# Performance work log

Hardware: AMD Instinct MI355X
Metric: run time of the kernel (lower is better)

The kernel has to match this reference:

```python
import jax, jax.numpy as jnp
import numpy as np


def _decode(out, anchors, t, case, thresh):
    # out: [B, 3*D, H, W] -> [B, H, W, 3, D]; D = 5 + n_classes
    B, C, H, W = out.shape
    o = jnp.transpose(out, (0, 2, 3, 1)).reshape(B, H, W, 3, C // 3)
    mask = o[..., 0] > thresh  # objectness logit threshold (pre-sigmoid, as in original)
    dt = out.dtype
    gx = jnp.arange(W, dtype=dt)  # grid x runs along W (index[:,2] in original)
    gy = jnp.arange(H, dtype=dt)  # grid y runs along H (index[:,1] in original)
    scale = t / case
    cx = (gx[None, None, :, None] + o[..., 1]) * scale
    cy = (gy[None, :, None, None] + o[..., 2]) * scale
    w = anchors[None, None, None, :, 0] * jnp.exp(o[..., 3]) / case
    h = anchors[None, None, None, :, 1] * jnp.exp(o[..., 4]) / case
    p = jax.nn.sigmoid(o[..., 0])
    cls_idx = jnp.argmax(o[..., 5:], axis=-1).astype(dt)
    boxes = jnp.stack([p, cx, cy, w, h, cls_idx], axis=-1).reshape(-1, 6)
    return boxes, mask.reshape(-1)


def setup_inputs() -> dict:
    key = jax.random.key(0)
    k13, k26, k52, kt = jax.random.split(key, 4)
    B = 32
    inp = {
        "output_13": jax.random.normal(k13, (B, 255, 13, 13), dtype=jnp.float32),
        "output_26": jax.random.normal(k26, (B, 255, 26, 26), dtype=jnp.float32),
        "output_52": jax.random.normal(k52, (B, 255, 52, 52), dtype=jnp.float32),
        # canonical YOLOv3 pixel anchors per scale
        "anchors_13": jnp.array([[116.0, 90.0], [156.0, 198.0], [373.0, 326.0]], dtype=jnp.float32),
        "anchors_26": jnp.array([[30.0, 61.0], [62.0, 45.0], [59.0, 119.0]], dtype=jnp.float32),
        "anchors_52": jnp.array([[10.0, 13.0], [16.0, 30.0], [33.0, 23.0]], dtype=jnp.float32),
        "thresh": jnp.array([0.5], dtype=jnp.float32),
        "case": 416,
    }
    return inp


def reference(output_13, output_26, output_52, anchors_13, anchors_26, anchors_52, thresh, case):
    th = thresh[0]
    b13, m13 = _decode(output_13, anchors_13, 32.0, case, th)
    b26, m26 = _decode(output_26, anchors_26, 16.0, case, th)
    b52, m52 = _decode(output_52, anchors_52, 8.0, case, th)
    boxes = jnp.concatenate([b13, b26, b52], axis=0)  # [N_total, 6], row-major (b,h,w,a) per scale
    mask = jnp.concatenate([m13, m26, m52], axis=0)   # boxes[mask] == original torch.cat output
    return boxes, mask
```

## Files before the change

kernel.cpp:

```cpp
#include <hip/hip_runtime.h>


#define NCLS 80

template<int HW, int W>
__device__ __forceinline__ void decode4(
    const float* __restrict__ in, const float* __restrict__ anch,
    float scale, float inv_case, float th,
    int a, int t, int row_base, int B,
    float* __restrict__ boxes, float* __restrict__ mask)
{
    if (t >= B * HW * 4) return;
    const int rt  = t >> 2;
    const int seg = t & 3;
    const int b   = rt / HW;
    const int hw  = rt - b * HW;

    const float* p = in + ((size_t)b * 255 + (size_t)a * 85) * HW + hw;

    const float* pc = p + (size_t)(5 + seg * 20) * HW;
    float v[20];
#pragma unroll
    for (int j = 0; j < 20; ++j)
        v[j] = __builtin_nontemporal_load(&pc[(size_t)j * HW]);

    float best = v[0];
    int   bi   = seg * 20;
#pragma unroll
    for (int j = 1; j < 20; ++j)
        if (v[j] > best) { best = v[j]; bi = seg * 20 + j; }

    float o0 = __builtin_nontemporal_load(&p[0 * (size_t)HW]);
    float o1 = __builtin_nontemporal_load(&p[1 * (size_t)HW]);
    float o2 = __builtin_nontemporal_load(&p[2 * (size_t)HW]);
    float o3 = __builtin_nontemporal_load(&p[3 * (size_t)HW]);
    float o4 = __builtin_nontemporal_load(&p[4 * (size_t)HW]);

#pragma unroll
    for (int m = 1; m <= 2; m <<= 1) {
        float ob = __shfl_xor(best, m);
        int   oi = __shfl_xor(bi,   m);
        if (ob > best || (ob == best && oi < bi)) { best = ob; bi = oi; }
    }

    if (seg == 0) {
        int h = hw / W;
        int w = hw - h * W;
        float px = 1.0f / (1.0f + __expf(-o0));
        float cx = ((float)w + o1) * scale;
        float cy = ((float)h + o2) * scale;
        float bw = anch[2 * a + 0] * __expf(o3) * inv_case;
        float bh = anch[2 * a + 1] * __expf(o4) * inv_case;

        int row = row_base + rt * 3 + a;
        float2* ob2 = reinterpret_cast<float2*>(boxes + (size_t)row * 6);
        ob2[0] = make_float2(px, cx);
        ob2[1] = make_float2(cy, bw);
        ob2[2] = make_float2(bh, (float)bi);
        mask[row] = (o0 > th) ? 1.0f : 0.0f;
    }
}

__global__ __launch_bounds__(256) void detector_kernel(
    const float* __restrict__ in13, const float* __restrict__ in26,
    const float* __restrict__ in52,
    const float* __restrict__ a13, const float* __restrict__ a26,
    const float* __restrict__ a52,
    const float* __restrict__ thp, const int* __restrict__ casep,
    float* __restrict__ boxes, float* __restrict__ mask,
    int B, int nb52, int nb26)
{
    const int a  = blockIdx.y;
    const int bx = blockIdx.x;
    const float th       = thp[0];
    const float inv_case = 1.0f / (float)casep[0];

    if (bx < nb52) {
        int t = bx * 256 + threadIdx.x;
        decode4<2704, 52>(in52, a52, 8.0f * inv_case, inv_case, th,
                          a, t, B * (169 + 676) * 3, B, boxes, mask);
    } else if (bx < nb52 + nb26) {
        int t = (bx - nb52) * 256 + threadIdx.x;
        decode4<676, 26>(in26, a26, 16.0f * inv_case, inv_case, th,
                         a, t, B * 169 * 3, B, boxes, mask);
    } else {
        int t = (bx - nb52 - nb26) * 256 + threadIdx.x;
        decode4<169, 13>(in13, a13, 32.0f * inv_case, inv_case, th,
                         a, t, 0, B, boxes, mask);
    }
}

extern "C" void kernel_launch(void* const* d_in, const int* in_sizes, int n_in,
                              void* d_out, int out_size, void* d_ws, size_t ws_size,
                              hipStream_t stream) {
    const float* in13 = (const float*)d_in[0];
    const float* in26 = (const float*)d_in[1];
    const float* in52 = (const float*)d_in[2];
    const float* a13  = (const float*)d_in[3];
    const float* a26  = (const float*)d_in[4];
    const float* a52  = (const float*)d_in[5];
    const float* thp  = (const float*)d_in[6];
    const int*   casep = (const int*)d_in[7];

    const int B = in_sizes[0] / (255 * 169);

    const int nb52 = (B * 2704 * 4 + 255) / 256;
    const int nb26 = (B * 676  * 4 + 255) / 256;
    const int nb13 = (B * 169  * 4 + 255) / 256;

    const int nrows = B * (169 + 676 + 2704) * 3;
    float* boxes = (float*)d_out;
    float* mask  = (float*)d_out + (size_t)nrows * 6;

    dim3 grid(nb52 + nb26 + nb13, 3);
    detector_kernel<<<grid, 256, 0, stream>>>(
        in13, in26, in52, a13, a26, a52, thp, casep,
        boxes, mask, B, nb52, nb26);
}
```

Before: 171.5 us.

## Split 52-scale decode into vectorized partial-argmax and merge kernels

Restructures the work into two kernels. The first computes per-class-chunk argmax partials for the 52 scale using float4 loads, writes them to workspace, and also fully decodes the 26 scale (with a shared-memory merge) and the 13 scale. The second kernel merges the four 52-scale partials and writes the boxes. The aim is wider, better-coalesced loads and more parallelism across class chunks, at the cost of an extra launch and a workspace round trip. Nontemporal loads are also dropped.

```diff
diff --git a/kernel.cpp b/kernel.cpp
--- a/kernel.cpp
+++ b/kernel.cpp
@@ -1,15 +1,146 @@
 #include <hip/hip_runtime.h>
 
 
-#define NCLS 80
-
-template<int HW, int W>
-__device__ __forceinline__ void decode4(
+typedef float vf4 __attribute__((ext_vector_type(4)));
+
+#define UPD1(B,I,V,C) { if ((V) > (B)) { (B)=(V); (I)=(C); } }
+#define UPD4(bb,ii,vv,cc) \
+    UPD1(bb.x, ii.x, vv.x, cc) UPD1(bb.y, ii.y, vv.y, cc) \
+    UPD1(bb.z, ii.z, vv.z, cc) UPD1(bb.w, ii.w, vv.w, cc)
+#define MRG1(B,I,V,C) { if ((V) > (B) || ((V)==(B) && (C) < (I))) { (B)=(V); (I)=(C); } }
+#define MRG4(bb,ii,vv,cc) \
+    MRG1(bb.x, ii.x, vv.x, cc.x) MRG1(bb.y, ii.y, vv.y, cc.y) \
+    MRG1(bb.z, ii.z, vv.z, cc.z) MRG1(bb.w, ii.w, vv.w, cc.w)
+
+__device__ __forceinline__ void store_p(float2* pb, int col, vf4 b, int4 i) {
+    vf4* p = reinterpret_cast<vf4*>(pb + (size_t)col * 4);
+    vf4 lo = {b.x, (float)i.x, b.y, (float)i.y};
+    vf4 hi = {b.z, (float)i.z, b.w, (float)i.w};
+    p[0] = lo; p[1] = hi;
+}
+
+__device__ __forceinline__ void p1_chunk52(
+    const float* __restrict__ in52, float2* __restrict__ partial, int u)
+{
+    const int slice = u >> 2;
+    const int k     = u & 3;
+    const int t     = threadIdx.x;
+    const vf4* __restrict__ cp = reinterpret_cast<const vf4*>(
+        in52 + (size_t)slice * 85 * 2704 + (size_t)(5 + 20 * k) * 2704);
+
+    const bool a2 = (t < 164);
+    const int base = 20 * k;
+
+    vf4 b0 = cp[t], b1 = cp[256 + t];
+    vf4 b2 = a2 ? cp[512 + t] : b0;
+    int4 i0 = {base, base, base, base}, i1 = i0, i2 = i0;
+
+    vf4 n0 = cp[676 + t], n1 = cp[676 + 256 + t];
+    vf4 n2 = a2 ? cp[676 + 512 + t] : n0;
+
+#pragma unroll 2
+    for (int c = 1; c < 19; ++c) {
+        const vf4* ch = cp + (size_t)(c + 1) * 676;
+        vf4 m0 = ch[t], m1 = ch[256 + t];
+        vf4 m2 = a2 ? ch[512 + t] : m0;
+        const int cls = base + c;
+        UPD4(b0, i0, n0, cls) UPD4(b1, i1, n1, cls) UPD4(b2, i2, n2, cls)
+        n0 = m0; n1 = m1; n2 = m2;
+    }
+    UPD4(b0, i0, n0, base + 19) UPD4(b1, i1, n1, base + 19) UPD4(b2, i2, n2, base + 19)
+
+    float2* pb = partial + (size_t)u * 2704;
+    store_p(pb, t, b0, i0);
+    store_p(pb, 256 + t, b1, i1);
+    if (a2) store_p(pb, 512 + t, b2, i2);
+}
+
+__device__ __forceinline__ void p1_full26(
+    const float* __restrict__ in26, const float* __restrict__ anch,
+    float scale, float inv_case, float th, int slice, int rb26,
+    float* __restrict__ boxes, float* __restrict__ mask,
+    vf4* __restrict__ lbest, int4* __restrict__ lbi)
+{
+    const int t = threadIdx.x;
+    const int b = slice / 3, a = slice - b * 3;
+    const vf4* __restrict__ sp = reinterpret_cast<const vf4*>(in26)
+                               + (size_t)slice * 85 * 169;
+    const vf4* __restrict__ cp = sp + 5 * 169;
+
+    const bool a2 = (t < 164);
+    const int p0 = t,        k40 = p0 / 169, c0 = p0 - k40 * 169;
+    const int p1 = 256 + t,  k41 = p1 / 169, c1 = p1 - k41 * 169;
+    const int p2 = 512 + t,  k42 = p2 / 169, c2 = p2 - k42 * 169;
+    (void)c0; (void)c1; (void)c2;
+
+    vf4 b0 = cp[p0], b1 = cp[p1];
+    vf4 b2 = a2 ? cp[p2] : b0;
+    int4 i0 = {k40, k40, k40, k40}, i1 = {k41, k41, k41, k41}, i2 = {k42, k42, k42, k42};
+
+    vf4 n0 = cp[676 + p0], n1 = cp[676 + p1];
+    vf4 n2 = a2 ? cp[676 + p2] : n0;
+
+#pragma unroll 2
+    for (int g = 1; g < 19; ++g) {
+        const vf4* gp = cp + (size_t)(g + 1) * 676;
+        vf4 m0 = gp[p0], m1 = gp[p1];
+        vf4 m2 = a2 ? gp[p2] : m0;
+        const int g4 = 4 * g;
+        UPD4(b0, i0, n0, g4 + k40) UPD4(b1, i1, n1, g4 + k41) UPD4(b2, i2, n2, g4 + k42)
+        n0 = m0; n1 = m1; n2 = m2;
+    }
+    UPD4(b0, i0, n0, 76 + k40) UPD4(b1, i1, n1, 76 + k41) UPD4(b2, i2, n2, 76 + k42)
+
+    lbest[p0] = b0; lbi[p0] = i0;
+    lbest[p1] = b1; lbi[p1] = i1;
+    if (a2) { lbest[p2] = b2; lbi[p2] = i2; }
+    __syncthreads();
+
+    if (t < 169) {
+        vf4 bb = lbest[t]; int4 ii = lbi[t];
+#pragma unroll
+        for (int k4 = 1; k4 < 4; ++k4) {
+            vf4 vb = lbest[k4 * 169 + t]; int4 vi = lbi[k4 * 169 + t];
+            MRG4(bb, ii, vb, vi)
+        }
+        vf4 o0 = sp[t], o1 = sp[169 + t], o2 = sp[2 * 169 + t];
+        vf4 o3 = sp[3 * 169 + t], o4 = sp[4 * 169 + t];
+        const float A0 = anch[2 * a + 0], A1 = anch[2 * a + 1];
+        const float e0[4] = {o0.x, o0.y, o0.z, o0.w};
+        const float e1[4] = {o1.x, o1.y, o1.z, o1.w};
+        const float e2[4] = {o2.x, o2.y, o2.z, o2.w};
+        const float e3[4] = {o3.x, o3.y, o3.z, o3.w};
+        const float e4[4] = {o4.x, o4.y, o4.z, o4.w};
+        const int   bi[4] = {ii.x, ii.y, ii.z, ii.w};
+        const float bv[4] = {bb.x, bb.y, bb.z, bb.w};
+        (void)bv;
+#pragma unroll
+        for (int e = 0; e < 4; ++e) {
+            const int hw = t * 4 + e;
+            const int hh = hw / 26;
+            const int ww = hw - hh * 26;
+            const float px = 1.f / (1.f + __expf(-e0[e]));
+            const float cx = ((float)ww + e1[e]) * scale;
+            const float cy = ((float)hh + e2[e]) * scale;
+            const float bw = A0 * __expf(e3[e]) * inv_case;
+            const float bh = A1 * __expf(e4[e]) * inv_case;
+            const int row = rb26 + (b * 676 + hw) * 3 + a;
+            float2* ob2 = reinterpret_cast<float2*>(boxes + (size_t)row * 6);
+            ob2[0] = make_float2(px, cx);
+            ob2[1] = make_float2(cy, bw);
+            ob2[2] = make_float2(bh, (float)bi[e]);
+            mask[row] = (e0[e] > th) ? 1.0f : 0.0f;
+        }
+    }
+}
+
+__device__ __forceinline__ void decode4_13(
     const float* __restrict__ in, const float* __restrict__ anch,
     float scale, float inv_case, float th,
-    int a, int t, int row_base, int B,
+    int a, int t, int B,
     float* __restrict__ boxes, float* __restrict__ mask)
 {
+    constexpr int HW = 169, W = 13;
     if (t >= B * HW * 4) return;
     const int rt  = t >> 2;
     const int seg = t & 3;
@@ -17,12 +148,10 @@
     const int hw  = rt - b * HW;
 
     const float* p = in + ((size_t)b * 255 + (size_t)a * 85) * HW + hw;
-
     const float* pc = p + (size_t)(5 + seg * 20) * HW;
     float v[20];
 #pragma unroll
-    for (int j = 0; j < 20; ++j)
-        v[j] = __builtin_nontemporal_load(&pc[(size_t)j * HW]);
+    for (int j = 0; j < 20; ++j) v[j] = pc[(size_t)j * HW];
 
     float best = v[0];
     int   bi   = seg * 20;
@@ -30,11 +159,8 @@
     for (int j = 1; j < 20; ++j)
         if (v[j] > best) { best = v[j]; bi = seg * 20 + j; }
 
-    float o0 = __builtin_nontemporal_load(&p[0 * (size_t)HW]);
-    float o1 = __builtin_nontemporal_load(&p[1 * (size_t)HW]);
-    float o2 = __builtin_nontemporal_load(&p[2 * (size_t)HW]);
-    float o3 = __builtin_nontemporal_load(&p[3 * (size_t)HW]);
-    float o4 = __builtin_nontemporal_load(&p[4 * (size_t)HW]);
+    float o0 = p[0 * (size_t)HW], o1 = p[1 * (size_t)HW], o2 = p[2 * (size_t)HW];
+    float o3 = p[3 * (size_t)HW], o4 = p[4 * (size_t)HW];
 
 #pragma unroll
     for (int m = 1; m <= 2; m <<= 1) {
@@ -44,15 +170,13 @@
     }
 
     if (seg == 0) {
-        int h = hw / W;
-        int w = hw - h * W;
-        float px = 1.0f / (1.0f + __expf(-o0));
-        float cx = ((float)w + o1) * scale;
-        float cy = ((float)h + o2) * scale;
-        float bw = anch[2 * a + 0] * __expf(o3) * inv_case;
-        float bh = anch[2 * a + 1] * __expf(o4) * inv_case;
-
-        int row = row_base + rt * 3 + a;
+        const int h = hw / W, w = hw - (hw / W) * W;
+        const float px = 1.0f / (1.0f + __expf(-o0));
+        const float cx = ((float)w + o1) * scale;
+        const float cy = ((float)h + o2) * scale;
+        const float bw = anch[2 * a + 0] * __expf(o3) * inv_case;
+        const float bh = anch[2 * a + 1] * __expf(o4) * inv_case;
+        const int row = rt * 3 + a;
         float2* ob2 = reinterpret_cast<float2*>(boxes + (size_t)row * 6);
         ob2[0] = make_float2(px, cx);
         ob2[1] = make_float2(cy, bw);
@@ -61,32 +185,91 @@
     }
 }
 
-__global__ __launch_bounds__(256) void detector_kernel(
+__global__ __launch_bounds__(256) void phase1_kernel(
     const float* __restrict__ in13, const float* __restrict__ in26,
     const float* __restrict__ in52,
     const float* __restrict__ a13, const float* __restrict__ a26,
-    const float* __restrict__ a52,
     const float* __restrict__ thp, const int* __restrict__ casep,
+    float2* __restrict__ partial,
     float* __restrict__ boxes, float* __restrict__ mask,
-    int B, int nb52, int nb26)
-{
-    const int a  = blockIdx.y;
-    const int bx = blockIdx.x;
-    const float th       = thp[0];
+    int B, int nb13)
+{
+    __shared__ vf4 lbest[676];
+    __shared__ int4 lbi[676];
+    const int gx = blockIdx.x;
+    const int n52c = B * 12, n26 = B * 3;
+
+    if (gx < n52c) { p1_chunk52(in52, partial, gx); return; }
+    if (gx < n52c + n26) {
+        const float inv_case = 1.0f / (float)casep[0];
+        p1_full26(in26, a26, 16.0f * inv_case, inv_case, thp[0],
+                  gx - n52c, B * 169 * 3, boxes, mask, lbest, lbi);
+        return;
+    }
+    const int u = gx - n52c - n26;
+    const int a = u / nb13;
+    const int t = (u - a * nb13) * 256 + threadIdx.x;
     const float inv_case = 1.0f / (float)casep[0];
-
-    if (bx < nb52) {
-        int t = bx * 256 + threadIdx.x;
-        decode4<2704, 52>(in52, a52, 8.0f * inv_case, inv_case, th,
-                          a, t, B * (169 + 676) * 3, B, boxes, mask);
-    } else if (bx < nb52 + nb26) {
-        int t = (bx - nb52) * 256 + threadIdx.x;
-        decode4<676, 26>(in26, a26, 16.0f * inv_case, inv_case, th,
-                         a, t, B * 169 * 3, B, boxes, mask);
-    } else {
-        int t = (bx - nb52 - nb26) * 256 + threadIdx.x;
-        decode4<169, 13>(in13, a13, 32.0f * inv_case, inv_case, th,
-                         a, t, 0, B, boxes, mask);
+    decode4_13(in13, a13, 32.0f * inv_case, inv_case, thp[0], a, t, B, boxes, mask);
+}
+
+__global__ __launch_bounds__(256) void phase2_kernel(
+    const float* __restrict__ in52, const float* __restrict__ a52,
+    const float* __restrict__ thp, const int* __restrict__ casep,
+    const float2* __restrict__ partial,
+    float* __restrict__ boxes, float* __restrict__ mask, int B)
+{
+    const int t = threadIdx.x;
+    if (t >= 169) return;
+    const int u = blockIdx.x;
+    const int slice = u >> 2, q = u & 3;
+    const int b = slice / 3, a = slice - b * 3;
+    const int col = q * 169 + t;
+    const float th = thp[0];
+    const float inv_case = 1.0f / (float)casep[0];
+    const float scale = 8.0f * inv_case;
+
+    const vf4* pp = reinterpret_cast<const vf4*>(partial + (size_t)slice * 4 * 2704);
+    vf4 e0 = pp[(size_t)col * 2], e1 = pp[(size_t)col * 2 + 1];
+    vf4 bb = {e0.x, e0.z, e1.x, e1.z};
+    int4 ii = {(int)e0.y, (int)e0.w, (int)e1.y, (int)e1.w};
+#pragma unroll
+    for (int k = 1; k < 4; ++k) {
+        vf4 f0 = pp[(size_t)k * 1352 + col * 2];
+        vf4 f1 = pp[(size_t)k * 1352 + col * 2 + 1];
+        vf4 vb = {f0.x, f0.z, f1.x, f1.z};
+        int4 vi = {(int)f0.y, (int)f0.w, (int)f1.y, (int)f1.w};
+        MRG4(bb, ii, vb, vi)
+    }
+
+    const vf4* sp = reinterpret_cast<const vf4*>(in52) + (size_t)slice * 85 * 676;
+    vf4 o0 = sp[col], o1 = sp[676 + col], o2 = sp[2 * 676 + col];
+    vf4 o3 = sp[3 * 676 + col], o4 = sp[4 * 676 + col];
+
+    const float A0 = a52[2 * a + 0], A1 = a52[2 * a + 1];
+    const int rb52 = B * (169 + 676) * 3;
+    const float e0a[4] = {o0.x, o0.y, o0.z, o0.w};
+    const float e1a[4] = {o1.x, o1.y, o1.z, o1.w};
+    const float e2a[4] = {o2.x, o2.y, o2.z, o2.w};
+    const float e3a[4] = {o3.x, o3.y, o3.z, o3.w};
+    const float e4a[4] = {o4.x, o4.y, o4.z, o4.w};
+    const int   bia[4] = {ii.x, ii.y, ii.z, ii.w};
+#pragma unroll
+    for (int e = 0; e < 4; ++e) {
+        const int hw = col * 4 + e;
+        const int hh = hw / 52;
+        const int ww = hw - hh * 52;
+        const float px = 1.f / (1.f + __expf(-e0a[e]));
+        const float cx = ((float)ww + e1a[e]) * scale;
+        const float cy = ((float)hh + e2a[e]) * scale;
+        const float bw = A0 * __expf(e3a[e]) * inv_case;
+        const float bh = A1 * __expf(e4a[e]) * inv_case;
+        const int row = rb52 + (b * 2704 + hw) * 3 + a;
+        float2* ob2 = reinterpret_cast<float2*>(boxes + (size_t)row * 6);
+        ob2[0] = make_float2(px, cx);
+        ob2[1] = make_float2(cy, bw);
+        ob2[2] = make_float2(bh, (float)bia[e]);
+        mask[row] = (e0a[e] > th) ? 1.0f : 0.0f;
     }
 }
 
@@ -103,17 +286,18 @@
     const int*   casep = (const int*)d_in[7];
 
     const int B = in_sizes[0] / (255 * 169);
-
-    const int nb52 = (B * 2704 * 4 + 255) / 256;
-    const int nb26 = (B * 676  * 4 + 255) / 256;
-    const int nb13 = (B * 169  * 4 + 255) / 256;
+    const int nb13 = (B * 169 * 4 + 255) / 256;
 
     const int nrows = B * (169 + 676 + 2704) * 3;
     float* boxes = (float*)d_out;
     float* mask  = (float*)d_out + (size_t)nrows * 6;
-
-    dim3 grid(nb52 + nb26 + nb13, 3);
-    detector_kernel<<<grid, 256, 0, stream>>>(
-        in13, in26, in52, a13, a26, a52, thp, casep,
-        boxes, mask, B, nb52, nb26);
-}
+    float2* partial = (float2*)d_ws;
+
+    dim3 g1(B * 12 + B * 3 + 3 * nb13);
+    phase1_kernel<<<g1, 256, 0, stream>>>(
+        in13, in26, in52, a13, a26, thp, casep, partial, boxes, mask, B, nb13);
+
+    dim3 g2(B * 12);
+    phase2_kernel<<<g2, 256, 0, stream>>>(
+        in52, a52, thp, casep, partial, boxes, mask, B);
+}
```

Result: slower. 181.1 us (+5.6%).
